# Optimization experiments

Measured on AMD Instinct MI355X. Metric: run time of the kernel, lower is better.

Reference implementation:

```python
import jax, jax.numpy as jnp
import numpy as np

GDEP = 3
ALPHA = 0.05
C_IN = 32
C_OUT = 32


def setup_inputs() -> dict:
    key = jax.random.key(0)
    k1, k2, k3, k4 = jax.random.split(key, 4)
    B, C, V, L = 16, C_IN, 512, 168
    x = jax.random.normal(k1, (B, C, V, L), dtype=jnp.float32)
    adj = jax.random.uniform(k2, (V, V), dtype=jnp.float32)
    fan_in = (GDEP + 1) * C_IN  # Conv2d 1x1: kaiming-uniform-ish init
    bound = 1.0 / np.sqrt(fan_in)
    W = jax.random.uniform(k3, (C_OUT, fan_in), minval=-bound, maxval=bound, dtype=jnp.float32)
    b = jax.random.uniform(k4, (C_OUT,), minval=-bound, maxval=bound, dtype=jnp.float32)
    return {"x": x, "adj": adj, "W": W, "b": b}


def reference(x, adj, W, b):
    V = adj.shape[0]
    a = adj + jnp.eye(V, dtype=adj.dtype)
    d = a.sum(axis=1)
    a = a / d[:, None]                      # row-normalized adjacency [V, V]
    h = x
    outs = [h]
    for _ in range(GDEP):                   # small fixed depth loop
        prop = jnp.einsum('ncvl,vw->ncwl', h, a)
        h = ALPHA * x + (1.0 - ALPHA) * prop
        outs.append(h)
    ho = jnp.concatenate(outs, axis=1)      # [B, (gdep+1)*C, V, L]
    # 1x1 conv == channel contraction
    out = jnp.einsum('bcvl,oc->bovl', ho, W) + b[None, :, None, None]
    return out
```

## Files before the change

### kernel.cpp

```cpp
#include <hip/hip_runtime.h>

#define V 512
#define L 168
#define PLANE 86016
#define CHSTRIDE 2752512
#define NFLAT 5376
#define B_ 16
#define HDRB (1u << 20)

typedef __attribute__((ext_vector_type(8))) short s16x8;
typedef __attribute__((ext_vector_type(4))) float f32x4;
typedef unsigned short u16;

__device__ inline short f2bf(float f) {
    unsigned u = __builtin_bit_cast(unsigned, f);
    u += 0x7FFF + ((u >> 16) & 1);
    return (short)(u >> 16);
}

__global__ __launch_bounds__(256) void prep_b(const float* __restrict__ adj,
                                              const float* __restrict__ W,
                                              u16* __restrict__ ATb,
                                              u16* __restrict__ Wb) {
    if (blockIdx.x == V) {
        const float al = 0.05f, be = 0.95f;
        for (int i = threadIdx.x; i < 1024; i += 256) {
            const int o = i >> 5, c = i & 31;
            const float w0 = W[o * 128 + c];
            const float w1 = W[o * 128 + 32 + c];
            const float w2 = W[o * 128 + 64 + c];
            const float w3 = W[o * 128 + 96 + c];
            Wb[o * 128 + c]      = f2bf(w0 + al * (w1 + w2 + w3));
            Wb[o * 128 + 32 + c] = f2bf(be * (w1 + al * (w2 + w3)));
            Wb[o * 128 + 64 + c] = f2bf(be * be * (w2 + al * w3));
            Wb[o * 128 + 96 + c] = f2bf(be * be * be * w3);
        }
        return;
    }
    const int v = blockIdx.x;
    float s = 0.f;
    for (int w = threadIdx.x; w < V; w += 256)
        s += adj[v * V + w] + (w == v ? 1.f : 0.f);
    __shared__ float red[256];
    red[threadIdx.x] = s;
    __syncthreads();
    for (int off = 128; off > 0; off >>= 1) {
        if ((int)threadIdx.x < off) red[threadIdx.x] += red[threadIdx.x + off];
        __syncthreads();
    }
    const float inv = 1.f / red[0];
    for (int w = threadIdx.x; w < V; w += 256)
        ATb[w * V + v] = f2bf((adj[v * V + w] + (w == v ? 1.f : 0.f)) * inv);
}

template <bool SRCF32>
__global__ __launch_bounds__(256, 2) void prop_p(const void* __restrict__ src,
                                                 const u16* __restrict__ ATb,
                                                 u16* __restrict__ dst) {
    const int b = blockIdx.z, w0 = blockIdx.y * 256, n0 = blockIdx.x * 64;
    const int tid = threadIdx.x, lane = tid & 63, wave = tid >> 6;
    const int colb = lane & 15, kg = lane >> 4;
    __shared__ u16 Hs[2][8 * 64 * 8];

    const int sn = tid & 63;
    const int sc = (n0 + sn) / L, sl = (n0 + sn) - sc * L;
    const size_t bH = (size_t)b * CHSTRIDE;
    const size_t srcCol = bH + (size_t)sc * PLANE + sl;

    f32x4 acc[4][4];
#pragma unroll
    for (int i = 0; i < 4; i++)
#pragma unroll
        for (int j = 0; j < 4; j++) acc[i][j] = (f32x4){0.f, 0.f, 0.f, 0.f};

    s16x8 t0, t1;
#define LOADT(v0base)                                                              \
    {                                                                              \
        _Pragma("unroll") for (int j = 0; j < 8; j++) {                            \
            const size_t o0 = srcCol + (size_t)((v0base) + wave * 8 + j) * L;      \
            const size_t o1 = srcCol + (size_t)((v0base) + 32 + wave * 8 + j) * L; \
            if (SRCF32) {                                                          \
                t0[j] = f2bf(((const float*)src)[o0]);                             \
                t1[j] = f2bf(((const float*)src)[o1]);                             \
            } else {                                                               \
                t0[j] = (short)((const u16*)src)[o0];                              \
                t1[j] = (short)((const u16*)src)[o1];                              \
            }                                                                      \
        }                                                                          \
    }

    LOADT(0);
    int buf = 0;
    for (int v0 = 0; v0 < V; v0 += 64) {
        *(s16x8*)&Hs[buf][wave * 512 + sn * 8] = t0;
        *(s16x8*)&Hs[buf][(wave + 4) * 512 + sn * 8] = t1;
        __syncthreads();
        if (v0 + 64 < V) LOADT(v0 + 64);
#pragma unroll
        for (int kk = 0; kk < 2; kk++) {
            s16x8 afr[4], bfr[4];
#pragma unroll
            for (int mt = 0; mt < 4; mt++)
                afr[mt] = *(const s16x8*)&ATb[(size_t)(w0 + wave * 64 + mt * 16 + colb) * V +
                                              v0 + kk * 32 + kg * 8];
#pragma unroll
            for (int nt = 0; nt < 4; nt++)
                bfr[nt] = *(const s16x8*)&Hs[buf][(kk * 4 + kg) * 512 + (nt * 16 + colb) * 8];
#pragma unroll
            for (int mt = 0; mt < 4; mt++)
#pragma unroll
                for (int nt = 0; nt < 4; nt++)
                    acc[mt][nt] = __builtin_amdgcn_mfma_f32_16x16x32_bf16(afr[mt], bfr[nt],
                                                                          acc[mt][nt], 0, 0, 0);
        }
        buf ^= 1;
    }
#undef LOADT

#pragma unroll
    for (int mt = 0; mt < 4; mt++) {
        const int wrow0 = w0 + wave * 64 + mt * 16 + kg * 4;
#pragma unroll
        for (int nt = 0; nt < 4; nt++) {
            const int ncol = n0 + nt * 16 + colb;
            const int c = ncol / L, l = ncol - c * L;
            const size_t base = bH + (size_t)c * PLANE + l;
#pragma unroll
            for (int r = 0; r < 4; r++)
                dst[base + (size_t)(wrow0 + r) * L] = f2bf(acc[mt][nt][r]);
        }
    }
}

__global__ __launch_bounds__(256) void outconv_b(const float* __restrict__ x,
                                                 const u16* __restrict__ p1,
                                                 const u16* __restrict__ p2,
                                                 const u16* __restrict__ p3,
                                                 const u16* __restrict__ Wb,
                                                 const float* __restrict__ bias,
                                                 float* __restrict__ out) {
    const int b = blockIdx.y, p0 = blockIdx.x * 64;
    const int tid = threadIdx.x, lane = tid & 63, wave = tid >> 6;
    const int colb = lane & 15, kg = lane >> 4;
    __shared__ u16 Hs[16 * 64 * 8];
    const size_t bH = (size_t)b * CHSTRIDE;
    const u16* bufs[4] = {nullptr, p1, p2, p3};

    {
        const int pos = tid & 63;
#pragma unroll
        for (int p = 0; p < 4; p++) {
            const int m = wave + p * 4;
            s16x8 t;
            if (p == 0) {
                const float* srcx = x + bH + (size_t)((m & 3) * 8) * PLANE + p0 + pos;
#pragma unroll
                for (int j = 0; j < 8; j++) t[j] = f2bf(srcx[(size_t)j * PLANE]);
            } else {
                const u16* srch = bufs[p] + bH + (size_t)((m & 3) * 8) * PLANE + p0 + pos;
#pragma unroll
                for (int j = 0; j < 8; j++) t[j] = (short)srch[(size_t)j * PLANE];
            }
            *(s16x8*)&Hs[m * 512 + pos * 8] = t;
        }
    }
    __syncthreads();

    f32x4 acc[2];
    acc[0] = (f32x4){0.f, 0.f, 0.f, 0.f};
    acc[1] = acc[0];
#pragma unroll
    for (int kk = 0; kk < 4; kk++) {
        const s16x8 bfr = *(const s16x8*)&Hs[(kk * 4 + kg) * 512 + (wave * 16 + colb) * 8];
#pragma unroll
        for (int mt = 0; mt < 2; mt++) {
            const s16x8 afr = *(const s16x8*)&Wb[(mt * 16 + colb) * 128 + kk * 32 + kg * 8];
            acc[mt] = __builtin_amdgcn_mfma_f32_16x16x32_bf16(afr, bfr, acc[mt], 0, 0, 0);
        }
    }
#pragma unroll
    for (int mt = 0; mt < 2; mt++)
#pragma unroll
        for (int r = 0; r < 4; r++) {
            const int o = mt * 16 + kg * 4 + r;
            out[bH + (size_t)o * PLANE + p0 + wave * 16 + colb] = bias[o] + acc[mt][r];
        }
}

extern "C" void kernel_launch(void* const* d_in, const int* in_sizes, int n_in,
                              void* d_out, int out_size, void* d_ws, size_t ws_size,
                              hipStream_t stream) {
    const float* x = (const float*)d_in[0];
    const float* adj = (const float*)d_in[1];
    const float* W = (const float*)d_in[2];
    const float* bias = (const float*)d_in[3];
    float* out = (float*)d_out;

    char* ws = (char*)d_ws;
    u16* ATb = (u16*)ws;
    u16* Wb = (u16*)(ws + 524288);
    u16* hbuf = (u16*)(ws + HDRB);

    prep_b<<<V + 1, 256, 0, stream>>>(adj, W, ATb, Wb);

    const size_t perBuf = (size_t)CHSTRIDE * 2;
    const size_t avail = ws_size > HDRB ? ws_size - HDRB : 0;
    int nbc = (int)(avail / (3 * perBuf));
    if (nbc < 1) nbc = 1;
    if (nbc > B_) nbc = B_;

    for (int b0 = 0; b0 < B_; b0 += nbc) {
        const int nb = (B_ - b0 < nbc) ? (B_ - b0) : nbc;
        const float* xb = x + (size_t)b0 * CHSTRIDE;
        float* outb = out + (size_t)b0 * CHSTRIDE;
        u16* p1 = hbuf;
        u16* p2 = hbuf + (size_t)nbc * CHSTRIDE;
        u16* p3 = hbuf + (size_t)2 * nbc * CHSTRIDE;

        const dim3 pg(NFLAT / 64, 2, nb);
        const dim3 og(PLANE / 64, nb);
        prop_p<true><<<pg, 256, 0, stream>>>((const void*)xb, ATb, p1);
        prop_p<false><<<pg, 256, 0, stream>>>((const void*)p1, ATb, p2);
        prop_p<false><<<pg, 256, 0, stream>>>((const void*)p2, ATb, p3);
        outconv_b<<<og, 256, 0, stream>>>(xb, p1, p2, p3, Wb, bias, outb);
    }
}
```

Measured before the change: 564.7 us.

## Store propagation intermediates V-contiguous and read GEMM operands directly from global

A new transpose kernel converts x to bf16 in a [B][C][L][V] layout, and every propagation output is written in that same layout. The propagation GEMM can then load its B operand as contiguous 16-byte vectors straight from global memory and store results as packed 4-element vectors. This replaces the earlier per-element strided loads, LDS staging and double buffering, and the output conv now also reads the transposed buffers. The costs are an extra transpose pass, a fourth workspace buffer that may force more batch chunks, strided final fp32 output writes, and redundant B-fragment loads across waves with no LDS reuse.

Result: slower. 868.3 us (+53.8%).

```diff
diff --git a/kernel.cpp b/kernel.cpp
--- a/kernel.cpp
+++ b/kernel.cpp
@@ -53,19 +53,39 @@
         ATb[w * V + v] = f2bf((adj[v * V + w] + (w == v ? 1.f : 0.f)) * inv);
 }
 
-template <bool SRCF32>
-__global__ __launch_bounds__(256, 2) void prop_p(const void* __restrict__ src,
+__global__ __launch_bounds__(256) void cvtT(const float* __restrict__ x,
+                                            u16* __restrict__ xa) {
+    const int b = blockIdx.z >> 5, c = blockIdx.z & 31;
+    const int v0 = blockIdx.y * 64, l0 = blockIdx.x * 64;
+    const int tid = threadIdx.x;
+    __shared__ float T[64][65];
+    const float* xp = x + (size_t)b * CHSTRIDE + (size_t)c * PLANE;
+    u16* xo = xa + (size_t)b * CHSTRIDE + (size_t)c * L * 512;
+
+#pragma unroll
+    for (int rep = 0; rep < 16; rep++) {
+        const int idx = rep * 256 + tid;
+        const int vv = idx >> 6, ll = idx & 63;
+        if (l0 + ll < L) T[vv][ll] = xp[(size_t)(v0 + vv) * L + l0 + ll];
+    }
+    __syncthreads();
+#pragma unroll
+    for (int rep = 0; rep < 16; rep++) {
+        const int idx = rep * 256 + tid;
+        const int ll = idx >> 6, vv = idx & 63;
+        if (l0 + ll < L)
+            xo[(size_t)(l0 + ll) * 512 + v0 + vv] = f2bf(T[vv][ll]);
+    }
+}
+
+__global__ __launch_bounds__(256, 2) void prop_g(const u16* __restrict__ src,
                                                  const u16* __restrict__ ATb,
                                                  u16* __restrict__ dst) {
     const int b = blockIdx.z, w0 = blockIdx.y * 256, n0 = blockIdx.x * 64;
     const int tid = threadIdx.x, lane = tid & 63, wave = tid >> 6;
     const int colb = lane & 15, kg = lane >> 4;
-    __shared__ u16 Hs[2][8 * 64 * 8];
-
-    const int sn = tid & 63;
-    const int sc = (n0 + sn) / L, sl = (n0 + sn) - sc * L;
-    const size_t bH = (size_t)b * CHSTRIDE;
-    const size_t srcCol = bH + (size_t)sc * PLANE + sl;
+    const size_t sB = (size_t)b * CHSTRIDE;
+    const u16* srcb = src + sB;
 
     f32x4 acc[4][4];
 #pragma unroll
@@ -73,95 +93,69 @@
 #pragma unroll
         for (int j = 0; j < 4; j++) acc[i][j] = (f32x4){0.f, 0.f, 0.f, 0.f};
 
-    s16x8 t0, t1;
-#define LOADT(v0base)                                                              \
-    {                                                                              \
-        _Pragma("unroll") for (int j = 0; j < 8; j++) {                            \
-            const size_t o0 = srcCol + (size_t)((v0base) + wave * 8 + j) * L;      \
-            const size_t o1 = srcCol + (size_t)((v0base) + 32 + wave * 8 + j) * L; \
-            if (SRCF32) {                                                          \
-                t0[j] = f2bf(((const float*)src)[o0]);                             \
-                t1[j] = f2bf(((const float*)src)[o1]);                             \
-            } else {                                                               \
-                t0[j] = (short)((const u16*)src)[o0];                              \
-                t1[j] = (short)((const u16*)src)[o1];                              \
-            }                                                                      \
-        }                                                                          \
-    }
-
-    LOADT(0);
-    int buf = 0;
-    for (int v0 = 0; v0 < V; v0 += 64) {
-        *(s16x8*)&Hs[buf][wave * 512 + sn * 8] = t0;
-        *(s16x8*)&Hs[buf][(wave + 4) * 512 + sn * 8] = t1;
-        __syncthreads();
-        if (v0 + 64 < V) LOADT(v0 + 64);
-#pragma unroll
-        for (int kk = 0; kk < 2; kk++) {
-            s16x8 afr[4], bfr[4];
-#pragma unroll
-            for (int mt = 0; mt < 4; mt++)
-                afr[mt] = *(const s16x8*)&ATb[(size_t)(w0 + wave * 64 + mt * 16 + colb) * V +
-                                              v0 + kk * 32 + kg * 8];
+    const int arow = w0 + wave * 64 + colb;
+    const int brow = n0 + colb;
+
+#pragma unroll 4
+    for (int kk = 0; kk < 16; kk++) {
+        const int v = kk * 32 + kg * 8;
+        s16x8 afr[4], bfr[4];
+#pragma unroll
+        for (int mt = 0; mt < 4; mt++)
+            afr[mt] = *(const s16x8*)&ATb[(size_t)(arow + mt * 16) * 512 + v];
+#pragma unroll
+        for (int nt = 0; nt < 4; nt++)
+            bfr[nt] = *(const s16x8*)&srcb[(size_t)(brow + nt * 16) * 512 + v];
+#pragma unroll
+        for (int mt = 0; mt < 4; mt++)
 #pragma unroll
             for (int nt = 0; nt < 4; nt++)
-                bfr[nt] = *(const s16x8*)&Hs[buf][(kk * 4 + kg) * 512 + (nt * 16 + colb) * 8];
-#pragma unroll
-            for (int mt = 0; mt < 4; mt++)
-#pragma unroll
-                for (int nt = 0; nt < 4; nt++)
-                    acc[mt][nt] = __builtin_amdgcn_mfma_f32_16x16x32_bf16(afr[mt], bfr[nt],
-                                                                          acc[mt][nt], 0, 0, 0);
-        }
-        buf ^= 1;
-    }
-#undef LOADT
+                acc[mt][nt] = __builtin_amdgcn_mfma_f32_16x16x32_bf16(afr[mt], bfr[nt],
+                                                                      acc[mt][nt], 0, 0, 0);
+    }
 
 #pragma unroll
     for (int mt = 0; mt < 4; mt++) {
-        const int wrow0 = w0 + wave * 64 + mt * 16 + kg * 4;
+        const int wrow = w0 + wave * 64 + mt * 16 + kg * 4;
 #pragma unroll
         for (int nt = 0; nt < 4; nt++) {
-            const int ncol = n0 + nt * 16 + colb;
-            const int c = ncol / L, l = ncol - c * L;
-            const size_t base = bH + (size_t)c * PLANE + l;
-#pragma unroll
-            for (int r = 0; r < 4; r++)
-                dst[base + (size_t)(wrow0 + r) * L] = f2bf(acc[mt][nt][r]);
-        }
-    }
-}
-
-__global__ __launch_bounds__(256) void outconv_b(const float* __restrict__ x,
+            ushort4 pk;
+            pk.x = (u16)f2bf(acc[mt][nt][0]);
+            pk.y = (u16)f2bf(acc[mt][nt][1]);
+            pk.z = (u16)f2bf(acc[mt][nt][2]);
+            pk.w = (u16)f2bf(acc[mt][nt][3]);
+            *(ushort4*)&dst[sB + (size_t)(n0 + nt * 16 + colb) * 512 + wrow] = pk;
+        }
+    }
+}
+
+__global__ __launch_bounds__(256) void outconv_g(const u16* __restrict__ xa,
                                                  const u16* __restrict__ p1,
                                                  const u16* __restrict__ p2,
                                                  const u16* __restrict__ p3,
                                                  const u16* __restrict__ Wb,
                                                  const float* __restrict__ bias,
                                                  float* __restrict__ out) {
-    const int b = blockIdx.y, p0 = blockIdx.x * 64;
+    const int b = blockIdx.y;
+    const int vt = blockIdx.x & 15, lt = blockIdx.x >> 4;
+    const int v0 = vt * 32, l0 = lt * 2;
     const int tid = threadIdx.x, lane = tid & 63, wave = tid >> 6;
     const int colb = lane & 15, kg = lane >> 4;
     __shared__ u16 Hs[16 * 64 * 8];
-    const size_t bH = (size_t)b * CHSTRIDE;
-    const u16* bufs[4] = {nullptr, p1, p2, p3};
+    const size_t sB = (size_t)b * CHSTRIDE;
+    const u16* bufs[4] = {xa, p1, p2, p3};
 
     {
-        const int pos = tid & 63;
+        const int pi = tid & 63;
+        const int v = v0 + (pi & 31), l = l0 + (pi >> 5);
 #pragma unroll
         for (int p = 0; p < 4; p++) {
             const int m = wave + p * 4;
+            const u16* srcp = bufs[p] + sB + (size_t)(wave * 8 * L + l) * 512 + v;
             s16x8 t;
-            if (p == 0) {
-                const float* srcx = x + bH + (size_t)((m & 3) * 8) * PLANE + p0 + pos;
-#pragma unroll
-                for (int j = 0; j < 8; j++) t[j] = f2bf(srcx[(size_t)j * PLANE]);
-            } else {
-                const u16* srch = bufs[p] + bH + (size_t)((m & 3) * 8) * PLANE + p0 + pos;
-#pragma unroll
-                for (int j = 0; j < 8; j++) t[j] = (short)srch[(size_t)j * PLANE];
-            }
-            *(s16x8*)&Hs[m * 512 + pos * 8] = t;
+#pragma unroll
+            for (int j = 0; j < 8; j++) t[j] = (short)srcp[(size_t)j * L * 512];
+            *(s16x8*)&Hs[m * 512 + pi * 8] = t;
         }
     }
     __syncthreads();
@@ -178,12 +172,15 @@
             acc[mt] = __builtin_amdgcn_mfma_f32_16x16x32_bf16(afr, bfr, acc[mt], 0, 0, 0);
         }
     }
+
+    const int pi = wave * 16 + colb;
+    const int v = v0 + (pi & 31), l = l0 + (pi >> 5);
 #pragma unroll
     for (int mt = 0; mt < 2; mt++)
 #pragma unroll
         for (int r = 0; r < 4; r++) {
             const int o = mt * 16 + kg * 4 + r;
-            out[bH + (size_t)o * PLANE + p0 + wave * 16 + colb] = bias[o] + acc[mt][r];
+            out[sB + (size_t)o * PLANE + (size_t)v * L + l] = bias[o] + acc[mt][r];
         }
 }
 
@@ -205,7 +202,7 @@
 
     const size_t perBuf = (size_t)CHSTRIDE * 2;
     const size_t avail = ws_size > HDRB ? ws_size - HDRB : 0;
-    int nbc = (int)(avail / (3 * perBuf));
+    int nbc = (int)(avail / (4 * perBuf));
     if (nbc < 1) nbc = 1;
     if (nbc > B_) nbc = B_;
 
@@ -213,15 +210,18 @@
         const int nb = (B_ - b0 < nbc) ? (B_ - b0) : nbc;
         const float* xb = x + (size_t)b0 * CHSTRIDE;
         float* outb = out + (size_t)b0 * CHSTRIDE;
-        u16* p1 = hbuf;
-        u16* p2 = hbuf + (size_t)nbc * CHSTRIDE;
-        u16* p3 = hbuf + (size_t)2 * nbc * CHSTRIDE;
+        u16* xa = hbuf;
+        u16* p1 = hbuf + (size_t)nbc * CHSTRIDE;
+        u16* p2 = hbuf + (size_t)2 * nbc * CHSTRIDE;
+        u16* p3 = hbuf + (size_t)3 * nbc * CHSTRIDE;
+
+        cvtT<<<dim3(3, 8, nb * 32), 256, 0, stream>>>(xb, xa);
 
         const dim3 pg(NFLAT / 64, 2, nb);
-        const dim3 og(PLANE / 64, nb);
-        prop_p<true><<<pg, 256, 0, stream>>>((const void*)xb, ATb, p1);
-        prop_p<false><<<pg, 256, 0, stream>>>((const void*)p1, ATb, p2);
-        prop_p<false><<<pg, 256, 0, stream>>>((const void*)p2, ATb, p3);
-        outconv_b<<<og, 256, 0, stream>>>(xb, p1, p2, p3, Wb, bias, outb);
-    }
-}
+        prop_g<<<pg, 256, 0, stream>>>(xa, ATb, p1);
+        prop_g<<<pg, 256, 0, stream>>>(p1, ATb, p2);
+        prop_g<<<pg, 256, 0, stream>>>(p2, ATb, p3);
+
+        outconv_g<<<dim3(16 * 84, nb), 256, 0, stream>>>(xa, p1, p2, p3, Wb, bias, outb);
+    }
+}
```

## Stage adjacency tile in padded LDS and drop H register prefetch

Applied to the files above, without the earlier changes.

The propagation kernel now copies a 256x64 tile of the transposed adjacency into padded shared memory each K-step, instead of having every wave read A fragments directly from global memory. The register double-buffered prefetch of the H tile is removed and replaced by a single LDS buffer with two barriers per iteration. The launch bound is raised to 3 blocks per CU. This is meant to cut redundant global and L2 traffic for A. In exchange it loses the overlap of global loads with MFMA work, adds a barrier per iteration, and uses more LDS per block.

Measured after the change: 537.1 us. 1.05x faster.

```diff
diff --git a/kernel.cpp b/kernel.cpp
--- a/kernel.cpp
+++ b/kernel.cpp
@@ -54,13 +54,14 @@
 }
 
 template <bool SRCF32>
-__global__ __launch_bounds__(256, 2) void prop_p(const void* __restrict__ src,
+__global__ __launch_bounds__(256, 3) void prop_s(const void* __restrict__ src,
                                                  const u16* __restrict__ ATb,
                                                  u16* __restrict__ dst) {
     const int b = blockIdx.z, w0 = blockIdx.y * 256, n0 = blockIdx.x * 64;
     const int tid = threadIdx.x, lane = tid & 63, wave = tid >> 6;
     const int colb = lane & 15, kg = lane >> 4;
-    __shared__ u16 Hs[2][8 * 64 * 8];
+    __shared__ u16 As[256 * 72];
+    __shared__ u16 Hs[8 * 64 * 8];
 
     const int sn = tid & 63;
     const int sc = (n0 + sn) / L, sl = (n0 + sn) - sc * L;
@@ -73,39 +74,45 @@
 #pragma unroll
         for (int j = 0; j < 4; j++) acc[i][j] = (f32x4){0.f, 0.f, 0.f, 0.f};
 
-    s16x8 t0, t1;
-#define LOADT(v0base)                                                              \
-    {                                                                              \
-        _Pragma("unroll") for (int j = 0; j < 8; j++) {                            \
-            const size_t o0 = srcCol + (size_t)((v0base) + wave * 8 + j) * L;      \
-            const size_t o1 = srcCol + (size_t)((v0base) + 32 + wave * 8 + j) * L; \
-            if (SRCF32) {                                                          \
-                t0[j] = f2bf(((const float*)src)[o0]);                             \
-                t1[j] = f2bf(((const float*)src)[o1]);                             \
-            } else {                                                               \
-                t0[j] = (short)((const u16*)src)[o0];                              \
-                t1[j] = (short)((const u16*)src)[o1];                              \
-            }                                                                      \
-        }                                                                          \
-    }
-
-    LOADT(0);
-    int buf = 0;
     for (int v0 = 0; v0 < V; v0 += 64) {
-        *(s16x8*)&Hs[buf][wave * 512 + sn * 8] = t0;
-        *(s16x8*)&Hs[buf][(wave + 4) * 512 + sn * 8] = t1;
         __syncthreads();
-        if (v0 + 64 < V) LOADT(v0 + 64);
+        {
+            const u16* ag = &ATb[(size_t)(w0 + tid) * 512 + v0];
+#pragma unroll
+            for (int q = 0; q < 8; q++) {
+                const s16x8 av = *(const s16x8*)(ag + q * 8);
+                *(s16x8*)((char*)As + tid * 144 + q * 16) = av;
+            }
+        }
+        {
+#pragma unroll
+            for (int h2 = 0; h2 < 2; h2++) {
+                const int koct = wave + h2 * 4;
+                s16x8 t;
+#pragma unroll
+                for (int j = 0; j < 8; j++) {
+                    const size_t off = srcCol + (size_t)(v0 + koct * 8 + j) * L;
+                    if (SRCF32)
+                        t[j] = f2bf(((const float*)src)[off]);
+                    else
+                        t[j] = (short)((const u16*)src)[off];
+                }
+                *(s16x8*)&Hs[koct * 512 + sn * 8] = t;
+            }
+        }
+        __syncthreads();
 #pragma unroll
         for (int kk = 0; kk < 2; kk++) {
+            const int cq = kk * 4 + kg;
             s16x8 afr[4], bfr[4];
 #pragma unroll
-            for (int mt = 0; mt < 4; mt++)
-                afr[mt] = *(const s16x8*)&ATb[(size_t)(w0 + wave * 64 + mt * 16 + colb) * V +
-                                              v0 + kk * 32 + kg * 8];
+            for (int mt = 0; mt < 4; mt++) {
+                const int wr = wave * 64 + mt * 16 + colb;
+                afr[mt] = *(const s16x8*)((const char*)As + wr * 144 + cq * 16);
+            }
 #pragma unroll
             for (int nt = 0; nt < 4; nt++)
-                bfr[nt] = *(const s16x8*)&Hs[buf][(kk * 4 + kg) * 512 + (nt * 16 + colb) * 8];
+                bfr[nt] = *(const s16x8*)&Hs[cq * 512 + (nt * 16 + colb) * 8];
 #pragma unroll
             for (int mt = 0; mt < 4; mt++)
 #pragma unroll
@@ -113,9 +120,7 @@
                     acc[mt][nt] = __builtin_amdgcn_mfma_f32_16x16x32_bf16(afr[mt], bfr[nt],
                                                                           acc[mt][nt], 0, 0, 0);
         }
-        buf ^= 1;
-    }
-#undef LOADT
+    }
 
 #pragma unroll
     for (int mt = 0; mt < 4; mt++) {
@@ -218,10 +223,10 @@
         u16* p3 = hbuf + (size_t)2 * nbc * CHSTRIDE;
 
         const dim3 pg(NFLAT / 64, 2, nb);
-        const dim3 og(PLANE / 64, nb);
-        prop_p<true><<<pg, 256, 0, stream>>>((const void*)xb, ATb, p1);
-        prop_p<false><<<pg, 256, 0, stream>>>((const void*)p1, ATb, p2);
-        prop_p<false><<<pg, 256, 0, stream>>>((const void*)p2, ATb, p3);
-        outconv_b<<<og, 256, 0, stream>>>(xb, p1, p2, p3, Wb, bias, outb);
-    }
-}
+        prop_s<true><<<pg, 256, 0, stream>>>((const void*)xb, ATb, p1);
+        prop_s<false><<<pg, 256, 0, stream>>>((const void*)p1, ATb, p2);
+        prop_s<false><<<pg, 256, 0, stream>>>((const void*)p2, ATb, p3);
+
+        outconv_b<<<dim3(PLANE / 64, nb), 256, 0, stream>>>(xb, p1, p2, p3, Wb, bias, outb);
+    }
+}
```
